# Performance work log

Measured on AMD Instinct MI355X. Metric: run time of the kernel, lower is better.

Reference implementation:

```python
import jax, jax.numpy as jnp
import numpy as np
import math

B, C, HH, WW = 4, 256, 64, 64
NUM_HEADS = 4
GROUPS = 8
EPS = 1e-5


def setup_inputs() -> dict:
    key = jax.random.key(0)
    k1, k2, k3 = jax.random.split(key, 3)
    x = jax.random.normal(k1, (B, C, HH, WW), dtype=jnp.float32)
    gn_w = jnp.ones((C,), dtype=jnp.float32)
    gn_b = jnp.zeros((C,), dtype=jnp.float32)
    qkv_w = jax.random.normal(k2, (3 * C, C), dtype=jnp.float32) * (1.0 / math.sqrt(C))
    qkv_b = jnp.zeros((3 * C,), dtype=jnp.float32)
    proj_w = jax.random.normal(k3, (C, C), dtype=jnp.float32) * (1.0 / math.sqrt(C))
    proj_b = jnp.zeros((C,), dtype=jnp.float32)
    return {"x": x, "gn_w": gn_w, "gn_b": gn_b, "qkv_w": qkv_w,
            "qkv_b": qkv_b, "proj_w": proj_w, "proj_b": proj_b}


def reference(x, gn_w, gn_b, qkv_w, qkv_b, proj_w, proj_b):
    b, c, h, w = x.shape
    nh = NUM_HEADS
    d = c // nh          # head dim = 64
    s = h * w            # sequence length = 4096

    # GroupNorm(8, c): normalize over (c//G, h, w) per group, biased variance
    xg = x.reshape(b, GROUPS, c // GROUPS, h, w)
    mu = xg.mean(axis=(2, 3, 4), keepdims=True)
    var = xg.var(axis=(2, 3, 4), keepdims=True)
    xn = ((xg - mu) * jax.lax.rsqrt(var + EPS)).reshape(b, c, h, w)
    xn = xn * gn_w[None, :, None, None] + gn_b[None, :, None, None]

    # 1x1 conv QKV == channel-wise matmul
    qkv = jnp.einsum('oc,bchw->bohw', qkv_w, xn) + qkv_b[None, :, None, None]
    qkv = qkv.reshape(b, 3, nh, d, s)
    q = jnp.transpose(qkv[:, 0], (0, 1, 3, 2))  # [b, nh, s, d]
    k = jnp.transpose(qkv[:, 1], (0, 1, 3, 2))
    v = jnp.transpose(qkv[:, 2], (0, 1, 3, 2))

    scale = 1.0 / math.sqrt(d)
    attn = jnp.einsum('bhqd,bhkd->bhqk', q, k) * scale  # [b, nh, s, s]
    attn = jax.nn.softmax(attn, axis=-1)
    out = jnp.einsum('bhqk,bhkd->bhqd', attn, v)        # [b, nh, s, d]

    out = jnp.transpose(out, (0, 1, 3, 2)).reshape(b, c, h, w)
    out = jnp.einsum('oc,bchw->bohw', proj_w, out) + proj_b[None, :, None, None]
    return out + x
```

## Files before the change

### kernel.cpp

```cpp
#include <hip/hip_runtime.h>
#include <hip/hip_bf16.h>

#define B_ 4
#define C_ 256
#define S_ 4096
#define NH_ 4
#define HD_ 64
#define LOG2E 1.4426950408889634f
#define QSC 0.18033688011112042f

typedef __attribute__((ext_vector_type(8))) short short8;
typedef __attribute__((ext_vector_type(4))) short short4v;
typedef __attribute__((ext_vector_type(4))) float f32x4;
typedef __attribute__((ext_vector_type(16))) float f32x16;
typedef __attribute__((ext_vector_type(4))) unsigned uint4v;

static __device__ __forceinline__ short f2bf(float f) {
  unsigned u = __builtin_bit_cast(unsigned, f);
  u += 0x7fffu + ((u >> 16) & 1u);
  return (short)(u >> 16);
}
static __device__ __forceinline__ float bf2f(short h) {
  unsigned u = ((unsigned)(unsigned short)h) << 16;
  return __builtin_bit_cast(float, u);
}

#if __has_builtin(__builtin_amdgcn_exp2f)
#define EXP2(x) __builtin_amdgcn_exp2f(x)
#else
#define EXP2(x) exp2f(x)
#endif

static __device__ __forceinline__ unsigned pkbf(float a, float b) {
  unsigned r;
  asm("v_cvt_pk_bf16_f32 %0, %1, %2" : "=v"(r) : "v"(a), "v"(b));
  return r;
}
static __device__ __forceinline__ void pl32swap(unsigned& a, unsigned& b) {
  asm volatile("v_permlane32_swap_b32 %0, %1" : "+v"(a), "+v"(b));
}
static __device__ __forceinline__ void gl_lds16(const short* g, char* l) {
  __builtin_amdgcn_global_load_lds(
      (const __attribute__((address_space(1))) void*)g,
      (__attribute__((address_space(3))) void*)l, 16, 0, 0);
}

__global__ __launch_bounds__(256) void k_pre(const float* __restrict__ x,
                                             const float* __restrict__ wq,
                                             const float* __restrict__ wp,
                                             float* __restrict__ part,
                                             short* __restrict__ oq,
                                             short* __restrict__ op) {
  int t = threadIdx.x;
  const float* p = x + (size_t)blockIdx.x * 16384;
  float s = 0.f, ss = 0.f;
  const float4* p4 = reinterpret_cast<const float4*>(p);
  for (int i = t; i < 4096; i += 256) {
    float4 v = p4[i];
    s += v.x + v.y + v.z + v.w;
    ss += v.x * v.x + v.y * v.y + v.z * v.z + v.w * v.w;
  }
  for (int m = 1; m < 64; m <<= 1) {
    s += __shfl_xor(s, m, 64);
    ss += __shfl_xor(ss, m, 64);
  }
  __shared__ float rs[4], rss[4];
  int w = t >> 6;
  if ((t & 63) == 0) { rs[w] = s; rss[w] = ss; }
  {
    int i = (blockIdx.x * 256 + t) * 4;
    const int n1 = 768 * 256;
    float sc = 1.f;
    const float* src;
    short* dst;
    if (i < n1) {
      src = wq + i; dst = oq + i;
      if (i < 256 * 256) sc = QSC;
    } else {
      src = wp + (i - n1); dst = op + (i - n1);
    }
    float4 v = *reinterpret_cast<const float4*>(src);
    short4v o;
    o[0] = f2bf(v.x * sc); o[1] = f2bf(v.y * sc);
    o[2] = f2bf(v.z * sc); o[3] = f2bf(v.w * sc);
    *reinterpret_cast<short4v*>(dst) = o;
  }
  __syncthreads();
  if (t == 0) {
    part[2 * blockIdx.x] = rs[0] + rs[1] + rs[2] + rs[3];
    part[2 * blockIdx.x + 1] = rss[0] + rss[1] + rss[2] + rss[3];
  }
}

__global__ __launch_bounds__(256) void k_gn_apply(const float* __restrict__ x,
                                                  const float* __restrict__ gw,
                                                  const float* __restrict__ gb,
                                                  const float* __restrict__ part,
                                                  short* __restrict__ xnt) {
  int st = blockIdx.x;
  int ct = blockIdx.y;
  int b = blockIdx.z;
  int t = threadIdx.x;
  __shared__ short T[64 * 72];
  __shared__ float smu[2], sri[2];
  int c0 = ct * 64, s0 = st * 64;
  if (t < 2) {
    int g = (c0 >> 5) + t;
    int base = b * 64 + g * 8;
    float s = 0.f, ss = 0.f;
    for (int j = 0; j < 8; j++) {
      s += part[2 * (base + j)];
      ss += part[2 * (base + j) + 1];
    }
    float inv = 1.f / (32.f * S_);
    float mu = s * inv;
    float var = ss * inv - mu * mu;
    smu[t] = mu;
    sri[t] = rsqrtf(var + 1e-5f);
  }
  __syncthreads();
  int r4 = t >> 4;
  int f4 = t & 15;
  for (int p = 0; p < 4; p++) {
    int r = p * 16 + r4;
    int c = c0 + r;
    int gl = r >> 5;
    float mu = smu[gl];
    float ri = sri[gl];
    float A = gw[c] * ri;
    float Bb = gb[c] - mu * A;
    float4 v = *reinterpret_cast<const float4*>(x + ((size_t)(b * C_ + c)) * S_ + s0 + f4 * 4);
    int sb = f4 * 4;
    T[(sb + 0) * 72 + r] = f2bf(v.x * A + Bb);
    T[(sb + 1) * 72 + r] = f2bf(v.y * A + Bb);
    T[(sb + 2) * 72 + r] = f2bf(v.z * A + Bb);
    T[(sb + 3) * 72 + r] = f2bf(v.w * A + Bb);
  }
  __syncthreads();
  for (int it = 0; it < 2; it++) {
    int cch = t + it * 256;
    int sl = cch >> 3, c8 = cch & 7;
    short8 v = *reinterpret_cast<short8*>(&T[sl * 72 + c8 * 8]);
    *reinterpret_cast<short8*>(xnt + ((size_t)(b * S_ + s0 + sl)) * C_ + c0 + c8 * 8) = v;
  }
}

template <int MODE, int NSP>
__global__ __launch_bounds__(256) void k_gemm(const short* __restrict__ Wbf,
                                              const short* __restrict__ Xt,
                                              const float* __restrict__ bias,
                                              const float* __restrict__ xres,
                                              short* __restrict__ q_sd,
                                              short* __restrict__ k_sd,
                                              short* __restrict__ v_ds,
                                              long op_stride,
                                              const float* __restrict__ lbufg,
                                              float* __restrict__ outp) {
  int tn = blockIdx.x;
  int tm = blockIdx.y;
  int b = blockIdx.z;
  int t = threadIdx.x;
  __shared__ short lds[4 * 64 * 72];
  char* glds = (char*)lds;
  int w = t >> 6, lane = t & 63;
  int wr = w >> 1, wc = w & 1;
  int l15 = lane & 15, l4 = lane >> 4;
  int wbg = __builtin_amdgcn_readfirstlane(w) << 10;

  f32x4 acc[4][4];
  for (int m = 0; m < 4; m++)
    for (int n = 0; n < 4; n++)
      for (int j = 0; j < 4; j++) acc[m][n][j] = 0.f;

  const short* Arow = Wbf + (size_t)(tm * 128) * 256;
  const short* Brow = Xt + ((size_t)b * S_ + tn * 128) * 256;

  int r0 = t >> 2, c40 = t & 3;
  int sw0 = (c40 ^ ((r0 >> 1) & 3)) * 8;
  int r1 = (t + 256) >> 2;
  int sw1 = (c40 ^ ((r1 >> 1) & 3)) * 8;

  if (MODE == 0) {
    gl_lds16(Arow + (size_t)r0 * 256 + sw0, glds + wbg);
    gl_lds16(Arow + (size_t)r1 * 256 + sw1, glds + 4096 + wbg);
    gl_lds16(Brow + (size_t)r0 * 256 + sw0, glds + 8192 + wbg);
    gl_lds16(Brow + (size_t)r1 * 256 + sw1, glds + 12288 + wbg);
    asm volatile("s_waitcnt vmcnt(0)" ::: "memory");
    __builtin_amdgcn_s_barrier();
    asm volatile("" ::: "memory");
    for (int step = 0; step < 8; step++) {
      char* cb = glds + ((step & 1) << 14);
      if (step + 1 < 8) {
        char* nb = glds + (((step + 1) & 1) << 14);
        int kk = (step + 1) * 32;
        gl_lds16(Arow + (size_t)r0 * 256 + kk + sw0, nb + wbg);
        gl_lds16(Arow + (size_t)r1 * 256 + kk + sw1, nb + 4096 + wbg);
        gl_lds16(Brow + (size_t)r0 * 256 + kk + sw0, nb + 8192 + wbg);
        gl_lds16(Brow + (size_t)r1 * 256 + kk + sw1, nb + 12288 + wbg);
      }
      short8 af[4], bf[4];
      for (int mt = 0; mt < 4; mt++) {
        int row = wr * 64 + mt * 16 + l15;
        af[mt] = *reinterpret_cast<short8*>(cb + row * 64 + ((l4 ^ ((row >> 1) & 3)) << 4));
      }
      for (int nt = 0; nt < 4; nt++) {
        int row = wc * 64 + nt * 16 + l15;
        bf[nt] = *reinterpret_cast<short8*>(cb + 8192 + row * 64 + ((l4 ^ ((row >> 1) & 3)) << 4));
      }
      for (int mt = 0; mt < 4; mt++)
        for (int nt = 0; nt < 4; nt++)
          acc[mt][nt] =
              __builtin_amdgcn_mfma_f32_16x16x32_bf16(af[mt], bf[nt], acc[mt][nt], 0, 0, 0);
      if (step + 1 < 8) {
        asm volatile("s_waitcnt vmcnt(0)" ::: "memory");
        __builtin_amdgcn_s_barrier();
        asm volatile("" ::: "memory");
      }
    }
  } else {
    short* Blp0 = lds + 8192;
    short* Blp1 = lds + 8192 + 5120;
#define MERGE_B(kk_, dstB)                                                     \
    do {                                                                       \
      for (int i = 0; i < 2; i++) {                                            \
        int cch = t + i * 256;                                                 \
        int r = cch >> 2, c4 = cch & 3;                                        \
        int c = (kk_) + c4 * 8;                                                \
        int bh2 = b * 4 + (c >> 6);                                            \
        int d = c & 63;                                                        \
        int s_glob = tn * 128 + r;                                             \
        size_t ro = ((size_t)bh2 * S_ + s_glob) * HD_ + d;                     \
        float a8[8] = {0.f, 0.f, 0.f, 0.f, 0.f, 0.f, 0.f, 0.f};                \
        float l = 0.f;                                                         \
        _Pragma("unroll") for (int i2 = 0; i2 < NSP; i2++) {                   \
          short8 pv = *reinterpret_cast<const short8*>(                        \
              Xt + (size_t)i2 * op_stride + ro);                               \
          _Pragma("unroll") for (int j = 0; j < 8; j++) a8[j] += bf2f(pv[j]);  \
          l += lbufg[(size_t)(i2 * 16 + bh2) * S_ + s_glob];                   \
        }                                                                      \
        float inv = 1.f / l;                                                   \
        short8 vbv;                                                            \
        _Pragma("unroll") for (int j = 0; j < 8; j++)                          \
            vbv[j] = f2bf(a8[j] * inv);                                        \
        *reinterpret_cast<short8*>(&(dstB)[r * 40 + c4 * 8]) = vbv;            \
      }                                                                        \
    } while (0)

    gl_lds16(Arow + (size_t)r0 * 256 + sw0, glds + wbg);
    gl_lds16(Arow + (size_t)r1 * 256 + sw1, glds + 4096 + wbg);
    MERGE_B(0, Blp0);
    __syncthreads();
    for (int step = 0; step < 8; step++) {
      char* cbA = glds + ((step & 1) ? 8192 : 0);
      short* cbB = (step & 1) ? Blp1 : Blp0;
      if (step + 1 < 8) {
        char* nbA = glds + (((step + 1) & 1) ? 8192 : 0);
        short* nbB = ((step + 1) & 1) ? Blp1 : Blp0;
        int kk = (step + 1) * 32;
        gl_lds16(Arow + (size_t)r0 * 256 + kk + sw0, nbA + wbg);
        gl_lds16(Arow + (size_t)r1 * 256 + kk + sw1, nbA + 4096 + wbg);
        MERGE_B(kk, nbB);
      }
      short8 af[4], bf[4];
      for (int mt = 0; mt < 4; mt++) {
        int row = wr * 64 + mt * 16 + l15;
        af[mt] = *reinterpret_cast<short8*>(cbA + row * 64 + ((l4 ^ ((row >> 1) & 3)) << 4));
      }
      for (int nt = 0; nt < 4; nt++) {
        int row = wc * 64 + nt * 16 + l15;
        bf[nt] = *reinterpret_cast<short8*>(&cbB[row * 40 + l4 * 8]);
      }
      for (int mt = 0; mt < 4; mt++)
        for (int nt = 0; nt < 4; nt++)
          acc[mt][nt] =
              __builtin_amdgcn_mfma_f32_16x16x32_bf16(af[mt], bf[nt], acc[mt][nt], 0, 0, 0);
      if (step + 1 < 8) __syncthreads();
    }
#undef MERGE_B
  }
  __syncthreads();

  if (MODE == 0) {
    int o_base = tm * 128 + wr * 64;
    int tt = o_base >> 8;
    int h = (o_base >> 6) & 3;
    int s_base = tn * 128 + wc * 64;
    int bh = b * NH_ + h;
    if (tt == 2) {
      for (int mt = 0; mt < 4; mt++)
        for (int nt = 0; nt < 4; nt++)
          for (int i = 0; i < 4; i++) {
            int o = o_base + mt * 16 + l4 * 4 + i;
            int dd = o & 63;
            int s = s_base + nt * 16 + l15;
            float val = acc[mt][nt][i] + bias[o];
            v_ds[((size_t)bh * HD_ + dd) * S_ + s] = f2bf(val);
          }
    } else {
      float bsc = (tt == 0) ? QSC : 1.f;
      short* T = lds + w * (64 * 72);
      for (int mt = 0; mt < 4; mt++)
        for (int nt = 0; nt < 4; nt++)
          for (int i = 0; i < 4; i++) {
            int o = o_base + mt * 16 + l4 * 4 + i;
            int dd = mt * 16 + l4 * 4 + i;
            int sl = nt * 16 + l15;
            float val = acc[mt][nt][i] + bias[o] * bsc;
            T[sl * 72 + dd] = f2bf(val);
          }
      short* dst = (tt == 0) ? q_sd : k_sd;
      for (int it = 0; it < 8; it++) {
        int cch = lane + it * 64;
        int sl = cch >> 3, c8 = cch & 7;
        short8 v = *reinterpret_cast<short8*>(&T[sl * 72 + c8 * 8]);
        *reinterpret_cast<short8*>(dst + ((size_t)bh * S_ + s_base + sl) * HD_ + c8 * 8) = v;
      }
    }
  } else {
    for (int mt = 0; mt < 4; mt++) {
      int o = tm * 128 + wr * 64 + mt * 16 + l4 * 4;
      for (int nt = 0; nt < 4; nt++) {
        int s = tn * 128 + wc * 64 + nt * 16 + l15;
        for (int i = 0; i < 4; i++) {
          size_t off = ((size_t)(b * C_ + o + i)) * S_ + s;
          outp[off] = acc[mt][nt][i] + bias[o + i] + xres[off];
        }
      }
    }
  }
}

__global__ __launch_bounds__(256, 2) void k_attn(const short* __restrict__ q_sd,
                                                 const short* __restrict__ k_sd,
                                                 const short* __restrict__ v_ds,
                                                 short* __restrict__ op_base,
                                                 long op_stride,
                                                 float* __restrict__ lbuf,
                                                 int ntile) {
  int bid = blockIdx.x;
  int qt = bid >> 5;
  int bh = (bid >> 1) & 15;
  int sk = bid & 1;
  int t = threadIdx.x, w = t >> 6, lane = t & 63;
  int l31 = lane & 31, hi = lane >> 5, hi8 = hi * 8;
  int qb = qt * 256 + w * 64;

  __shared__ char smem[49152];

  int wb = __builtin_amdgcn_readfirstlane(w) << 10;

  int r8 = t >> 3, s8 = t & 7;
  int sw8 = (s8 ^ (r8 & 7)) * 8;
  const short* kb = k_sd + ((size_t)bh * S_ + (size_t)sk * ntile * 64) * HD_;
  const short* vbg = v_ds + (size_t)bh * HD_ * S_ + sk * ntile * 64;
  int koff0 = r8 * 64 + sw8;
  int koff1 = koff0 + 32 * 64;
  size_t voff0 = (size_t)r8 * S_ + sw8;
  size_t voff1 = voff0 + (size_t)32 * S_;

#define STAGE(bsel, ti)                                                        \
  do {                                                                         \
    const short* kt_ = kb + (size_t)(ti) * (64 * HD_);                         \
    const short* vt_ = vbg + (ti) * 64;                                        \
    char* lb_ = smem + ((bsel) << 14) + wb;                                    \
    gl_lds16(kt_ + koff0, lb_);                                                \
    gl_lds16(kt_ + koff1, lb_ + 4096);                                         \
    gl_lds16(vt_ + voff0, lb_ + 8192);                                         \
    gl_lds16(vt_ + voff1, lb_ + 12288);                                        \
  } while (0)

  const short* qpA = q_sd + ((size_t)bh * S_ + qb + l31) * HD_ + hi8;
  short8 qfA[4], qfB[4];
#pragma unroll
  for (int sl = 0; sl < 4; sl++) {
    qfA[sl] = *reinterpret_cast<const short8*>(qpA + sl * 16);
    qfB[sl] = *reinterpret_cast<const short8*>(qpA + 32 * HD_ + sl * 16);
  }

  const short one_bf = (short)0x3F80;
  short8 eA, eB;
#pragma unroll
  for (int j = 0; j < 8; j++) {
    eA[j] = (l31 == 0) ? one_bf : (short)0;
    eB[j] = (l31 == 1) ? one_bf : (short)0;
  }

  int x7 = l31 & 7;
  int rb0 = l31 * 128;

  f32x16 OA0, OA1, OB0, OB1, lacc;
#pragma unroll
  for (int r = 0; r < 16; r++) {
    OA0[r] = 0.f; OA1[r] = 0.f; OB0[r] = 0.f; OB1[r] = 0.f; lacc[r] = 0.f;
  }

  STAGE(0, 0);
  if (ntile > 1) STAGE(1, 1);
  asm volatile("s_waitcnt vmcnt(4)" ::: "memory");
  __builtin_amdgcn_s_barrier();
  asm volatile("" ::: "memory");

#define MKPA2(pa0, pa1, s)                                                     \
  do {                                                                         \
    unsigned c0 = pkbf(s[0], s[1]), c1 = pkbf(s[2], s[3]);                     \
    unsigned c2 = pkbf(s[4], s[5]), c3 = pkbf(s[6], s[7]);                     \
    pl32swap(c0, c2); pl32swap(c1, c3);                                        \
    uint4v u0; u0[0] = c0; u0[1] = c1; u0[2] = c2; u0[3] = c3;                 \
    pa0 = __builtin_bit_cast(short8, u0);                                      \
    unsigned c4 = pkbf(s[8], s[9]), c5 = pkbf(s[10], s[11]);                   \
    unsigned c6 = pkbf(s[12], s[13]), c7 = pkbf(s[14], s[15]);                 \
    pl32swap(c4, c6); pl32swap(c5, c7);                                        \
    uint4v u1; u1[0] = c4; u1[1] = c5; u1[2] = c6; u1[3] = c7;                 \
    pa1 = __builtin_bit_cast(short8, u1);                                      \
  } while (0)

  int cs = 0;
  for (int it = 0; it < ntile; it++) {
    char* cur = smem + (cs << 14);
    int ns = (cs == 2) ? 0 : cs + 1;
    int ps = (cs == 0) ? 2 : cs - 1;
    if (it + 2 < ntile) STAGE(ps, it + 2);

    f32x16 sA0, sB0;
#pragma unroll
    for (int r = 0; r < 16; r++) { sA0[r] = 0.f; sB0[r] = 0.f; }
    __builtin_amdgcn_s_setprio(1);
#pragma unroll
    for (int sl = 0; sl < 4; sl++) {
      int so = ((sl * 2 + hi) ^ x7) << 4;
      short8 kf0 = *reinterpret_cast<short8*>(cur + rb0 + so);
      sA0 = __builtin_amdgcn_mfma_f32_32x32x16_bf16(kf0, qfA[sl], sA0, 0, 0, 0);
      sB0 = __builtin_amdgcn_mfma_f32_32x32x16_bf16(kf0, qfB[sl], sB0, 0, 0, 0);
    }

    f32x16 sA1, sB1;
#pragma unroll
    for (int r = 0; r < 16; r++) { sA1[r] = 0.f; sB1[r] = 0.f; }
#pragma unroll
    for (int sl = 0; sl < 4; sl++) {
      int so = ((sl * 2 + hi) ^ x7) << 4;
      short8 kf1 = *reinterpret_cast<short8*>(cur + 4096 + rb0 + so);
      sA1 = __builtin_amdgcn_mfma_f32_32x32x16_bf16(kf1, qfA[sl], sA1, 0, 0, 0);
      sB1 = __builtin_amdgcn_mfma_f32_32x32x16_bf16(kf1, qfB[sl], sB1, 0, 0, 0);
#pragma unroll
      for (int j = 0; j < 4; j++) {
        sA0[sl * 4 + j] = EXP2(sA0[sl * 4 + j]);
        sB0[sl * 4 + j] = EXP2(sB0[sl * 4 + j]);
      }
    }
    __builtin_amdgcn_s_setprio(0);

    short8 paA0, paA1, paB0, paB1;
    MKPA2(paA0, paA1, sA0);
    MKPA2(paB0, paB1, sB0);
    lacc = __builtin_amdgcn_mfma_f32_32x32x16_bf16(eA, paA0, lacc, 0, 0, 0);
    lacc = __builtin_amdgcn_mfma_f32_32x32x16_bf16(eA, paA1, lacc, 0, 0, 0);
    lacc = __builtin_amdgcn_mfma_f32_32x32x16_bf16(eB, paB0, lacc, 0, 0, 0);
    lacc = __builtin_amdgcn_mfma_f32_32x32x16_bf16(eB, paB1, lacc, 0, 0, 0);

    __builtin_amdgcn_s_setprio(1);
#pragma unroll
    for (int ks = 0; ks < 2; ks++) {
      int so = ((ks * 2 + hi) ^ x7) << 4;
      short8 vf0 = *reinterpret_cast<short8*>(cur + 8192 + rb0 + so);
      short8 vf1 = *reinterpret_cast<short8*>(cur + 12288 + rb0 + so);
      short8 pA = ks ? paA1 : paA0;
      short8 pB = ks ? paB1 : paB0;
      OA0 = __builtin_amdgcn_mfma_f32_32x32x16_bf16(vf0, pA, OA0, 0, 0, 0);
      OB0 = __builtin_amdgcn_mfma_f32_32x32x16_bf16(vf0, pB, OB0, 0, 0, 0);
      OA1 = __builtin_amdgcn_mfma_f32_32x32x16_bf16(vf1, pA, OA1, 0, 0, 0);
      OB1 = __builtin_amdgcn_mfma_f32_32x32x16_bf16(vf1, pB, OB1, 0, 0, 0);
#pragma unroll
      for (int j = 0; j < 8; j++) {
        sA1[ks * 8 + j] = EXP2(sA1[ks * 8 + j]);
        sB1[ks * 8 + j] = EXP2(sB1[ks * 8 + j]);
      }
    }
    __builtin_amdgcn_s_setprio(0);

    short8 paA2, paA3, paB2, paB3;
    MKPA2(paA2, paA3, sA1);
    MKPA2(paB2, paB3, sB1);
    lacc = __builtin_amdgcn_mfma_f32_32x32x16_bf16(eA, paA2, lacc, 0, 0, 0);
    lacc = __builtin_amdgcn_mfma_f32_32x32x16_bf16(eA, paA3, lacc, 0, 0, 0);
    lacc = __builtin_amdgcn_mfma_f32_32x32x16_bf16(eB, paB2, lacc, 0, 0, 0);
    lacc = __builtin_amdgcn_mfma_f32_32x32x16_bf16(eB, paB3, lacc, 0, 0, 0);

    __builtin_amdgcn_s_setprio(1);
#pragma unroll
    for (int ks = 2; ks < 4; ks++) {
      int so = ((ks * 2 + hi) ^ x7) << 4;
      short8 vf0 = *reinterpret_cast<short8*>(cur + 8192 + rb0 + so);
      short8 vf1 = *reinterpret_cast<short8*>(cur + 12288 + rb0 + so);
      short8 pA = (ks == 2) ? paA2 : paA3;
      short8 pB = (ks == 2) ? paB2 : paB3;
      OA0 = __builtin_amdgcn_mfma_f32_32x32x16_bf16(vf0, pA, OA0, 0, 0, 0);
      OB0 = __builtin_amdgcn_mfma_f32_32x32x16_bf16(vf0, pB, OB0, 0, 0, 0);
      OA1 = __builtin_amdgcn_mfma_f32_32x32x16_bf16(vf1, pA, OA1, 0, 0, 0);
      OB1 = __builtin_amdgcn_mfma_f32_32x32x16_bf16(vf1, pB, OB1, 0, 0, 0);
    }
    __builtin_amdgcn_s_setprio(0);

    if (it + 1 < ntile) {
      if (it + 2 < ntile)
        asm volatile("s_waitcnt vmcnt(4)" ::: "memory");
      else
        asm volatile("s_waitcnt vmcnt(0)" ::: "memory");
      __builtin_amdgcn_s_barrier();
      asm volatile("" ::: "memory");
    }
    cs = ns;
  }

  short* optrA = op_base + (size_t)sk * op_stride + ((size_t)bh * S_ + qb + l31) * HD_;
  short* optrB = optrA + 32 * HD_;
#pragma unroll
  for (int qd = 0; qd < 4; qd++) {
    short4v a0, a1, b0v, b1v;
#pragma unroll
    for (int i = 0; i < 4; i++) {
      a0[i] = f2bf(OA0[qd * 4 + i]);
      a1[i] = f2bf(OA1[qd * 4 + i]);
      b0v[i] = f2bf(OB0[qd * 4 + i]);
      b1v[i] = f2bf(OB1[qd * 4 + i]);
    }
    int d0 = qd * 8 + hi * 4;
    *reinterpret_cast<short4v*>(optrA + d0) = a0;
    *reinterpret_cast<short4v*>(optrA + 32 + d0) = a1;
    *reinterpret_cast<short4v*>(optrB + d0) = b0v;
    *reinterpret_cast<short4v*>(optrB + 32 + d0) = b1v;
  }
  if (hi == 0) {
    lbuf[(size_t)(sk * 16 + bh) * S_ + qb + l31] = lacc[0];
    lbuf[(size_t)(sk * 16 + bh) * S_ + qb + 32 + l31] = lacc[1];
  }
#undef STAGE
#undef MKPA2
}

extern "C" void kernel_launch(void* const* d_in, const int* in_sizes, int n_in,
                              void* d_out, int out_size, void* d_ws, size_t ws_size,
                              hipStream_t stream) {
  const float* x      = (const float*)d_in[0];
  const float* gn_w   = (const float*)d_in[1];
  const float* gn_b   = (const float*)d_in[2];
  const float* qkv_w  = (const float*)d_in[3];
  const float* qkv_b  = (const float*)d_in[4];
  const float* proj_w = (const float*)d_in[5];
  const float* proj_b = (const float*)d_in[6];
  char* ws = (char*)d_ws;
  float* part  = (float*)(ws + 2048);
  short* wqkv  = (short*)(ws + 4096);
  short* wproj = (short*)(ws + 397312);
  short* xnt   = (short*)(ws + 528384);
  short* q_sd  = (short*)(ws + 8916992);
  short* k_sd  = (short*)(ws + 17305600);
  short* v_ds  = (short*)(ws + 25694208);
  short* op_base = xnt;
  long op_stride = (42471424 - 528384) / 2;
  float* lbuf  = (float*)(ws + 50860032);
  float* outp  = (float*)d_out;

  k_pre<<<256, 256, 0, stream>>>(x, qkv_w, proj_w, part, wqkv, wproj);
  k_gn_apply<<<dim3(64, 4, 4), 256, 0, stream>>>(x, gn_w, gn_b, part, xnt);
  k_gemm<0, 0><<<dim3(32, 6, 4), 256, 0, stream>>>(wqkv, xnt, qkv_b, nullptr, q_sd, k_sd, v_ds,
                                                   0, nullptr, nullptr);
  k_attn<<<512, 256, 0, stream>>>(q_sd, k_sd, v_ds, op_base, op_stride, lbuf, 32);
  k_gemm<1, 2><<<dim3(32, 2, 4), 256, 0, stream>>>(wproj, op_base, proj_b, x, nullptr, nullptr,
                                                   nullptr, op_stride, lbuf, outp);
}
```

Measured before the change: 122.9 us.

## Process two KV tiles per barrier with a four-slot LDS ring

Replaces the three-slot LDS ring, which waited and hit a barrier after every 64-key tile, with a four-slot ring. Each loop iteration prefetches the next two tiles, computes two tiles back to back, then does one full vmcnt(0) wait and one barrier. The aim is to halve the number of barriers and waits in the attention main loop. In exchange, LDS per block rises to 64KB, which could limit occupancy, and the wait is now a full drain. The loop also assumes ntile is even.

```diff
diff --git a/kernel.cpp b/kernel.cpp
--- a/kernel.cpp
+++ b/kernel.cpp
@@ -345,7 +345,7 @@
   int l31 = lane & 31, hi = lane >> 5, hi8 = hi * 8;
   int qb = qt * 256 + w * 64;
 
-  __shared__ char smem[49152];
+  __shared__ char smem[65536];
 
   int wb = __builtin_amdgcn_readfirstlane(w) << 10;
 
@@ -396,7 +396,7 @@
 
   STAGE(0, 0);
   if (ntile > 1) STAGE(1, 1);
-  asm volatile("s_waitcnt vmcnt(4)" ::: "memory");
+  asm volatile("s_waitcnt vmcnt(0)" ::: "memory");
   __builtin_amdgcn_s_barrier();
   asm volatile("" ::: "memory");
 
@@ -414,102 +414,92 @@
     pa1 = __builtin_bit_cast(short8, u1);                                      \
   } while (0)
 
-  int cs = 0;
-  for (int it = 0; it < ntile; it++) {
-    char* cur = smem + (cs << 14);
-    int ns = (cs == 2) ? 0 : cs + 1;
-    int ps = (cs == 0) ? 2 : cs - 1;
-    if (it + 2 < ntile) STAGE(ps, it + 2);
-
-    f32x16 sA0, sB0;
-#pragma unroll
-    for (int r = 0; r < 16; r++) { sA0[r] = 0.f; sB0[r] = 0.f; }
-    __builtin_amdgcn_s_setprio(1);
-#pragma unroll
-    for (int sl = 0; sl < 4; sl++) {
-      int so = ((sl * 2 + hi) ^ x7) << 4;
-      short8 kf0 = *reinterpret_cast<short8*>(cur + rb0 + so);
-      sA0 = __builtin_amdgcn_mfma_f32_32x32x16_bf16(kf0, qfA[sl], sA0, 0, 0, 0);
-      sB0 = __builtin_amdgcn_mfma_f32_32x32x16_bf16(kf0, qfB[sl], sB0, 0, 0, 0);
-    }
-
-    f32x16 sA1, sB1;
-#pragma unroll
-    for (int r = 0; r < 16; r++) { sA1[r] = 0.f; sB1[r] = 0.f; }
-#pragma unroll
-    for (int sl = 0; sl < 4; sl++) {
-      int so = ((sl * 2 + hi) ^ x7) << 4;
-      short8 kf1 = *reinterpret_cast<short8*>(cur + 4096 + rb0 + so);
-      sA1 = __builtin_amdgcn_mfma_f32_32x32x16_bf16(kf1, qfA[sl], sA1, 0, 0, 0);
-      sB1 = __builtin_amdgcn_mfma_f32_32x32x16_bf16(kf1, qfB[sl], sB1, 0, 0, 0);
-#pragma unroll
-      for (int j = 0; j < 4; j++) {
-        sA0[sl * 4 + j] = EXP2(sA0[sl * 4 + j]);
-        sB0[sl * 4 + j] = EXP2(sB0[sl * 4 + j]);
-      }
-    }
-    __builtin_amdgcn_s_setprio(0);
-
-    short8 paA0, paA1, paB0, paB1;
-    MKPA2(paA0, paA1, sA0);
-    MKPA2(paB0, paB1, sB0);
-    lacc = __builtin_amdgcn_mfma_f32_32x32x16_bf16(eA, paA0, lacc, 0, 0, 0);
-    lacc = __builtin_amdgcn_mfma_f32_32x32x16_bf16(eA, paA1, lacc, 0, 0, 0);
-    lacc = __builtin_amdgcn_mfma_f32_32x32x16_bf16(eB, paB0, lacc, 0, 0, 0);
-    lacc = __builtin_amdgcn_mfma_f32_32x32x16_bf16(eB, paB1, lacc, 0, 0, 0);
-
-    __builtin_amdgcn_s_setprio(1);
-#pragma unroll
-    for (int ks = 0; ks < 2; ks++) {
-      int so = ((ks * 2 + hi) ^ x7) << 4;
-      short8 vf0 = *reinterpret_cast<short8*>(cur + 8192 + rb0 + so);
-      short8 vf1 = *reinterpret_cast<short8*>(cur + 12288 + rb0 + so);
-      short8 pA = ks ? paA1 : paA0;
-      short8 pB = ks ? paB1 : paB0;
-      OA0 = __builtin_amdgcn_mfma_f32_32x32x16_bf16(vf0, pA, OA0, 0, 0, 0);
-      OB0 = __builtin_amdgcn_mfma_f32_32x32x16_bf16(vf0, pB, OB0, 0, 0, 0);
-      OA1 = __builtin_amdgcn_mfma_f32_32x32x16_bf16(vf1, pA, OA1, 0, 0, 0);
-      OB1 = __builtin_amdgcn_mfma_f32_32x32x16_bf16(vf1, pB, OB1, 0, 0, 0);
-#pragma unroll
-      for (int j = 0; j < 8; j++) {
-        sA1[ks * 8 + j] = EXP2(sA1[ks * 8 + j]);
-        sB1[ks * 8 + j] = EXP2(sB1[ks * 8 + j]);
-      }
-    }
-    __builtin_amdgcn_s_setprio(0);
-
-    short8 paA2, paA3, paB2, paB3;
-    MKPA2(paA2, paA3, sA1);
-    MKPA2(paB2, paB3, sB1);
-    lacc = __builtin_amdgcn_mfma_f32_32x32x16_bf16(eA, paA2, lacc, 0, 0, 0);
-    lacc = __builtin_amdgcn_mfma_f32_32x32x16_bf16(eA, paA3, lacc, 0, 0, 0);
-    lacc = __builtin_amdgcn_mfma_f32_32x32x16_bf16(eB, paB2, lacc, 0, 0, 0);
-    lacc = __builtin_amdgcn_mfma_f32_32x32x16_bf16(eB, paB3, lacc, 0, 0, 0);
-
-    __builtin_amdgcn_s_setprio(1);
-#pragma unroll
-    for (int ks = 2; ks < 4; ks++) {
-      int so = ((ks * 2 + hi) ^ x7) << 4;
-      short8 vf0 = *reinterpret_cast<short8*>(cur + 8192 + rb0 + so);
-      short8 vf1 = *reinterpret_cast<short8*>(cur + 12288 + rb0 + so);
-      short8 pA = (ks == 2) ? paA2 : paA3;
-      short8 pB = (ks == 2) ? paB2 : paB3;
-      OA0 = __builtin_amdgcn_mfma_f32_32x32x16_bf16(vf0, pA, OA0, 0, 0, 0);
-      OB0 = __builtin_amdgcn_mfma_f32_32x32x16_bf16(vf0, pB, OB0, 0, 0, 0);
-      OA1 = __builtin_amdgcn_mfma_f32_32x32x16_bf16(vf1, pA, OA1, 0, 0, 0);
-      OB1 = __builtin_amdgcn_mfma_f32_32x32x16_bf16(vf1, pB, OB1, 0, 0, 0);
-    }
-    __builtin_amdgcn_s_setprio(0);
-
-    if (it + 1 < ntile) {
-      if (it + 2 < ntile)
-        asm volatile("s_waitcnt vmcnt(4)" ::: "memory");
-      else
-        asm volatile("s_waitcnt vmcnt(0)" ::: "memory");
+#define TILE_BODY(cur)                                                         \
+  do {                                                                         \
+    f32x16 sA0, sB0;                                                           \
+    _Pragma("unroll") for (int r = 0; r < 16; r++) { sA0[r] = 0.f; sB0[r] = 0.f; } \
+    __builtin_amdgcn_s_setprio(1);                                             \
+    _Pragma("unroll") for (int sl = 0; sl < 4; sl++) {                         \
+      int so = ((sl * 2 + hi) ^ x7) << 4;                                      \
+      short8 kf0 = *reinterpret_cast<short8*>((cur) + rb0 + so);               \
+      sA0 = __builtin_amdgcn_mfma_f32_32x32x16_bf16(kf0, qfA[sl], sA0, 0, 0, 0); \
+      sB0 = __builtin_amdgcn_mfma_f32_32x32x16_bf16(kf0, qfB[sl], sB0, 0, 0, 0); \
+    }                                                                          \
+    f32x16 sA1, sB1;                                                           \
+    _Pragma("unroll") for (int r = 0; r < 16; r++) { sA1[r] = 0.f; sB1[r] = 0.f; } \
+    _Pragma("unroll") for (int sl = 0; sl < 4; sl++) {                         \
+      int so = ((sl * 2 + hi) ^ x7) << 4;                                      \
+      short8 kf1 = *reinterpret_cast<short8*>((cur) + 4096 + rb0 + so);        \
+      sA1 = __builtin_amdgcn_mfma_f32_32x32x16_bf16(kf1, qfA[sl], sA1, 0, 0, 0); \
+      sB1 = __builtin_amdgcn_mfma_f32_32x32x16_bf16(kf1, qfB[sl], sB1, 0, 0, 0); \
+      _Pragma("unroll") for (int j = 0; j < 4; j++) {                          \
+        sA0[sl * 4 + j] = EXP2(sA0[sl * 4 + j]);                               \
+        sB0[sl * 4 + j] = EXP2(sB0[sl * 4 + j]);                               \
+      }                                                                        \
+    }                                                                          \
+    __builtin_amdgcn_s_setprio(0);                                             \
+    short8 paA0, paA1, paB0, paB1;                                             \
+    MKPA2(paA0, paA1, sA0);                                                    \
+    MKPA2(paB0, paB1, sB0);                                                    \
+    lacc = __builtin_amdgcn_mfma_f32_32x32x16_bf16(eA, paA0, lacc, 0, 0, 0);   \
+    lacc = __builtin_amdgcn_mfma_f32_32x32x16_bf16(eA, paA1, lacc, 0, 0, 0);   \
+    lacc = __builtin_amdgcn_mfma_f32_32x32x16_bf16(eB, paB0, lacc, 0, 0, 0);   \
+    lacc = __builtin_amdgcn_mfma_f32_32x32x16_bf16(eB, paB1, lacc, 0, 0, 0);   \
+    __builtin_amdgcn_s_setprio(1);                                             \
+    _Pragma("unroll") for (int ks = 0; ks < 2; ks++) {                         \
+      int so = ((ks * 2 + hi) ^ x7) << 4;                                      \
+      short8 vf0 = *reinterpret_cast<short8*>((cur) + 8192 + rb0 + so);        \
+      short8 vf1 = *reinterpret_cast<short8*>((cur) + 12288 + rb0 + so);       \
+      short8 pA = ks ? paA1 : paA0;                                            \
+      short8 pB = ks ? paB1 : paB0;                                            \
+      OA0 = __builtin_amdgcn_mfma_f32_32x32x16_bf16(vf0, pA, OA0, 0, 0, 0);    \
+      OB0 = __builtin_amdgcn_mfma_f32_32x32x16_bf16(vf0, pB, OB0, 0, 0, 0);    \
+      OA1 = __builtin_amdgcn_mfma_f32_32x32x16_bf16(vf1, pA, OA1, 0, 0, 0);    \
+      OB1 = __builtin_amdgcn_mfma_f32_32x32x16_bf16(vf1, pB, OB1, 0, 0, 0);    \
+      _Pragma("unroll") for (int j = 0; j < 8; j++) {                          \
+        sA1[ks * 8 + j] = EXP2(sA1[ks * 8 + j]);                               \
+        sB1[ks * 8 + j] = EXP2(sB1[ks * 8 + j]);                               \
+      }                                                                        \
+    }                                                                          \
+    __builtin_amdgcn_s_setprio(0);                                             \
+    short8 paA2, paA3, paB2, paB3;                                             \
+    MKPA2(paA2, paA3, sA1);                                                    \
+    MKPA2(paB2, paB3, sB1);                                                    \
+    lacc = __builtin_amdgcn_mfma_f32_32x32x16_bf16(eA, paA2, lacc, 0, 0, 0);   \
+    lacc = __builtin_amdgcn_mfma_f32_32x32x16_bf16(eA, paA3, lacc, 0, 0, 0);   \
+    lacc = __builtin_amdgcn_mfma_f32_32x32x16_bf16(eB, paB2, lacc, 0, 0, 0);   \
+    lacc = __builtin_amdgcn_mfma_f32_32x32x16_bf16(eB, paB3, lacc, 0, 0, 0);   \
+    __builtin_amdgcn_s_setprio(1);                                             \
+    _Pragma("unroll") for (int ks = 2; ks < 4; ks++) {                         \
+      int so = ((ks * 2 + hi) ^ x7) << 4;                                      \
+      short8 vf0 = *reinterpret_cast<short8*>((cur) + 8192 + rb0 + so);        \
+      short8 vf1 = *reinterpret_cast<short8*>((cur) + 12288 + rb0 + so);       \
+      short8 pA = (ks == 2) ? paA2 : paA3;                                     \
+      short8 pB = (ks == 2) ? paB2 : paB3;                                     \
+      OA0 = __builtin_amdgcn_mfma_f32_32x32x16_bf16(vf0, pA, OA0, 0, 0, 0);    \
+      OB0 = __builtin_amdgcn_mfma_f32_32x32x16_bf16(vf0, pB, OB0, 0, 0, 0);    \
+      OA1 = __builtin_amdgcn_mfma_f32_32x32x16_bf16(vf1, pA, OA1, 0, 0, 0);    \
+      OB1 = __builtin_amdgcn_mfma_f32_32x32x16_bf16(vf1, pB, OB1, 0, 0, 0);    \
+    }                                                                          \
+    __builtin_amdgcn_s_setprio(0);                                             \
+  } while (0)
+
+  int nit = ntile >> 1;
+  for (int j = 0; j < nit; j++) {
+    int t0 = 2 * j;
+    if (j + 1 < nit) {
+      STAGE((t0 + 2) & 3, t0 + 2);
+      STAGE((t0 + 3) & 3, t0 + 3);
+    }
+    char* cur0 = smem + ((t0 & 3) << 14);
+    char* cur1 = smem + (((t0 + 1) & 3) << 14);
+    TILE_BODY(cur0);
+    TILE_BODY(cur1);
+    if (j + 1 < nit) {
+      asm volatile("s_waitcnt vmcnt(0)" ::: "memory");
       __builtin_amdgcn_s_barrier();
       asm volatile("" ::: "memory");
     }
-    cs = ns;
   }
 
   short* optrA = op_base + (size_t)sk * op_stride + ((size_t)bh * S_ + qb + l31) * HD_;
@@ -536,6 +526,7 @@
   }
 #undef STAGE
 #undef MKPA2
+#undef TILE_BODY
 }
 
 extern "C" void kernel_launch(void* const* d_in, const int* in_sizes, int n_in,
```

After: 123.3 us. Within noise of the previous version (+0.3%).
